# Kernel tuning notes

Hardware: AMD Instinct MI355X
Metric: run time of the kernel (lower is better)

## Reference

```python
import jax, jax.numpy as jnp
import numpy as np

B, N, D = 8, 2048, 512   # batch, ctx_size, input_size
P, H = 16, 32            # num_pers, hidden_size


def setup_inputs() -> dict:
    key = jax.random.key(0)
    k1, k2 = jax.random.split(key)
    context = jax.random.normal(k1, (B, N, D), dtype=jnp.float32)
    # stacked weights of the 16 bias-free nn.Linear(input_size, hidden_size) layers
    # xavier-uniform-style scale: sqrt(6/(fan_in+fan_out))
    limit = np.sqrt(6.0 / (D + H)).astype(np.float32)
    W = jax.random.uniform(k2, (P, H, D), dtype=jnp.float32, minval=-limit, maxval=limit)
    ctx_mask = jnp.ones((B, N), dtype=jnp.int32)
    return {"context": context, "W": W, "ctx_mask": ctx_mask}


def reference(context, W, ctx_mask):
    # per-persona projection + relu: [P, B, N, H]
    fc = jax.nn.relu(jnp.einsum('bnd,phd->pbnh', context, W))
    # sum over personas of fc @ fc^T, then average: [B, N, N]
    att = jnp.einsum('pbnh,pbmh->bnm', fc, fc) / P
    # NOTE: original uses F.softmax(attention, dim=1) -> softmax over rows (axis=1)
    att = jax.nn.softmax(att, axis=1)
    # masked_fill with markoff_value=0 on masked columns then masked rows
    m = ctx_mask.astype(att.dtype)          # [B, N]
    att = att * m[:, None, :] * m[:, :, None]
    return att
```

## Files before the change

kernel.cpp:

```cpp
#include <hip/hip_runtime.h>

#define Bc 8
#define Nc 2048
#define Dc 512
#define PH 512
#define NN 4194304

#define BM 128
#define BN 128
#define BK 32

typedef __attribute__((ext_vector_type(8))) short bf16x8;
typedef __attribute__((ext_vector_type(4))) float f32x4;

static __device__ __forceinline__ unsigned short f2b(float x) {
    union { float f; unsigned u; } v; v.f = x;
    unsigned r = v.u + 0x7fffu + ((v.u >> 16) & 1u);
    return (unsigned short)(r >> 16);
}

static __device__ __forceinline__ void load16_lds(const unsigned short* g, unsigned short* l) {
    __builtin_amdgcn_global_load_lds(
        (const __attribute__((address_space(1))) void*)g,
        (__attribute__((address_space(3))) void*)l,
        16, 0, 0);
}

__global__ __launch_bounds__(256) void prep_kernel(
    const float* __restrict__ ctx, const float* __restrict__ W,
    unsigned short* __restrict__ Xb, unsigned short* __restrict__ Wb,
    float* __restrict__ rsum) {
    int t = blockIdx.x * 256 + threadIdx.x;
    if (t < 2097152) {
        float4 v = ((const float4*)ctx)[t];
        ushort4 o;
        o.x = f2b(v.x); o.y = f2b(v.y); o.z = f2b(v.z); o.w = f2b(v.w);
        ((ushort4*)Xb)[t] = o;
    }
    if (t < 65536) {
        float4 v = ((const float4*)W)[t];
        ushort4 o;
        o.x = f2b(v.x); o.y = f2b(v.y); o.z = f2b(v.z); o.w = f2b(v.w);
        ((ushort4*)Wb)[t] = o;
    }
    if (t < 4096) {
        float4 z; z.x = 0.f; z.y = 0.f; z.z = 0.f; z.w = 0.f;
        ((float4*)rsum)[t] = z;
    }
}

__global__ __launch_bounds__(256) void gemm1_relu(
    const unsigned short* __restrict__ Xb, const unsigned short* __restrict__ Wb,
    unsigned short* __restrict__ F) {
    __shared__ unsigned short As[BM * BK];
    __shared__ unsigned short Bs[BN * BK];
    const int tid = threadIdx.x;
    const int lane = tid & 63;
    const int wave = tid >> 6;
    const int wm = wave >> 1, wn = wave & 1;
    const int row0 = blockIdx.y * BM;
    const int col0 = blockIdx.x * BN;

    f32x4 acc[4][4] = {};

    for (int k0 = 0; k0 < Dc; k0 += BK) {
#pragma unroll
        for (int j = 0; j < 2; ++j) {
            int e = j * 256 + tid;
            int rr = e >> 2, cc = e & 3;
            load16_lds(&Xb[(size_t)(row0 + rr) * Dc + k0 + cc * 8], &As[e * 8]);
            load16_lds(&Wb[(size_t)(col0 + rr) * Dc + k0 + cc * 8], &Bs[e * 8]);
        }
        __syncthreads();

        bf16x8 af[4], bfr[4];
#pragma unroll
        for (int i = 0; i < 4; ++i) {
            af[i]  = *(const bf16x8*)&As[(wm * 64 + i * 16 + (lane & 15)) * BK + (lane >> 4) * 8];
            bfr[i] = *(const bf16x8*)&Bs[(wn * 64 + i * 16 + (lane & 15)) * BK + (lane >> 4) * 8];
        }
#pragma unroll
        for (int mi = 0; mi < 4; ++mi)
#pragma unroll
            for (int ni = 0; ni < 4; ++ni)
                acc[mi][ni] = __builtin_amdgcn_mfma_f32_16x16x32_bf16(af[mi], bfr[ni], acc[mi][ni], 0, 0, 0);
        __syncthreads();
    }

#pragma unroll
    for (int mi = 0; mi < 4; ++mi) {
#pragma unroll
        for (int ni = 0; ni < 4; ++ni) {
            int col  = col0 + wn * 64 + ni * 16 + (lane & 15);
            int rowb = row0 + wm * 64 + mi * 16 + ((lane >> 4) << 2);
#pragma unroll
            for (int r = 0; r < 4; ++r) {
                float v = fmaxf(acc[mi][ni][r], 0.0f);
                F[(size_t)(rowb + r) * PH + col] = f2b(v);
            }
        }
    }
}

__global__ __launch_bounds__(256) void gemm2_rsum(
    const unsigned short* __restrict__ F, float* __restrict__ rsum) {
    __shared__ unsigned short As[BM * BK];
    __shared__ unsigned short Bs[BN * BK];
    const int tid = threadIdx.x;
    const int lane = tid & 63;
    const int wave = tid >> 6;
    const int wm = wave >> 1, wn = wave & 1;
    const int b = blockIdx.y;

    int idx = blockIdx.x;
    int j = 0;
    while (((j + 1) * (j + 2) / 2) <= idx) ++j;
    int i = idx - j * (j + 1) / 2;
    const int row0 = i * BM;
    const int col0 = j * BN;
    const unsigned short* Fb = F + (size_t)b * Nc * PH;

    f32x4 acc[4][4] = {};

    for (int k0 = 0; k0 < PH; k0 += BK) {
#pragma unroll
        for (int jj = 0; jj < 2; ++jj) {
            int e = jj * 256 + tid;
            int rr = e >> 2, cc = e & 3;
            load16_lds(&Fb[(size_t)(row0 + rr) * PH + k0 + cc * 8], &As[e * 8]);
            load16_lds(&Fb[(size_t)(col0 + rr) * PH + k0 + cc * 8], &Bs[e * 8]);
        }
        __syncthreads();

        bf16x8 af[4], bfr[4];
#pragma unroll
        for (int q = 0; q < 4; ++q) {
            af[q]  = *(const bf16x8*)&As[(wm * 64 + q * 16 + (lane & 15)) * BK + (lane >> 4) * 8];
            bfr[q] = *(const bf16x8*)&Bs[(wn * 64 + q * 16 + (lane & 15)) * BK + (lane >> 4) * 8];
        }
#pragma unroll
        for (int mi = 0; mi < 4; ++mi)
#pragma unroll
            for (int ni = 0; ni < 4; ++ni)
                acc[mi][ni] = __builtin_amdgcn_mfma_f32_16x16x32_bf16(af[mi], bfr[ni], acc[mi][ni], 0, 0, 0);
        __syncthreads();
    }

    float csum[4] = {0.f, 0.f, 0.f, 0.f};
    float rsm[4][4];
#pragma unroll
    for (int mi = 0; mi < 4; ++mi)
#pragma unroll
        for (int r = 0; r < 4; ++r) rsm[mi][r] = 0.f;

#pragma unroll
    for (int mi = 0; mi < 4; ++mi) {
#pragma unroll
        for (int ni = 0; ni < 4; ++ni) {
#pragma unroll
            for (int r = 0; r < 4; ++r) {
                float e = __expf(acc[mi][ni][r] * 0.0625f - 32.0f);
                csum[ni] += e;
                rsm[mi][r] += e;
            }
        }
    }
#pragma unroll
    for (int ni = 0; ni < 4; ++ni) {
        float s = csum[ni];
        s += __shfl_xor(s, 16);
        s += __shfl_xor(s, 32);
        if ((lane >> 4) == 0)
            atomicAdd(&rsum[b * Nc + col0 + wn * 64 + ni * 16 + lane], s);
    }
    if (i != j) {
#pragma unroll
        for (int mi = 0; mi < 4; ++mi) {
#pragma unroll
            for (int r = 0; r < 4; ++r) {
                float s = rsm[mi][r];
                s += __shfl_xor(s, 1);
                s += __shfl_xor(s, 2);
                s += __shfl_xor(s, 4);
                s += __shfl_xor(s, 8);
                if ((lane & 15) == 0)
                    atomicAdd(&rsum[b * Nc + row0 + wm * 64 + mi * 16 + ((lane >> 4) << 2) + r], s);
            }
        }
    }
}

__global__ __launch_bounds__(256) void invr_kernel(
    const float* __restrict__ rsum, const int* __restrict__ mask,
    float* __restrict__ invr) {
    int t = blockIdx.x * 256 + threadIdx.x;
    if (t < Bc * Nc) invr[t] = (float)mask[t] / rsum[t];
}

__global__ __launch_bounds__(256) void gemm2_write_sym(
    const unsigned short* __restrict__ F, const float* __restrict__ invr,
    const int* __restrict__ mask, float* __restrict__ out) {
    __shared__ unsigned short As[BM * BK];
    __shared__ unsigned short Bs[BN * BK];
    __shared__ float Ts[32 * 132];
    const int tid = threadIdx.x;
    const int lane = tid & 63;
    const int wave = tid >> 6;
    const int wm = wave >> 1, wn = wave & 1;
    const int l15 = lane & 15, q = lane >> 4;
    const int b = blockIdx.y;

    int idx = blockIdx.x;
    int j = 0;
    while (((j + 1) * (j + 2) / 2) <= idx) ++j;
    int i = idx - j * (j + 1) / 2;
    const int row0 = i * BM;
    const int col0 = j * BN;
    const unsigned short* Fb = F + (size_t)b * Nc * PH;

    f32x4 acc[4][4] = {};

    for (int k0 = 0; k0 < PH; k0 += BK) {
#pragma unroll
        for (int jj = 0; jj < 2; ++jj) {
            int e = jj * 256 + tid;
            int rr = e >> 2, cc = e & 3;
            load16_lds(&Fb[(size_t)(row0 + rr) * PH + k0 + cc * 8], &As[e * 8]);
            load16_lds(&Fb[(size_t)(col0 + rr) * PH + k0 + cc * 8], &Bs[e * 8]);
        }
        __syncthreads();

        bf16x8 af[4], bfr[4];
#pragma unroll
        for (int qq = 0; qq < 4; ++qq) {
            af[qq]  = *(const bf16x8*)&As[(wm * 64 + qq * 16 + l15) * BK + q * 8];
            bfr[qq] = *(const bf16x8*)&Bs[(wn * 64 + qq * 16 + l15) * BK + q * 8];
        }
#pragma unroll
        for (int mi = 0; mi < 4; ++mi)
#pragma unroll
            for (int ni = 0; ni < 4; ++ni)
                acc[mi][ni] = __builtin_amdgcn_mfma_f32_16x16x32_bf16(af[mi], bfr[ni], acc[mi][ni], 0, 0, 0);
        __syncthreads();
    }

#pragma unroll
    for (int mi = 0; mi < 4; ++mi)
#pragma unroll
        for (int ni = 0; ni < 4; ++ni)
#pragma unroll
            for (int r = 0; r < 4; ++r)
                acc[mi][ni][r] = __expf(acc[mi][ni][r] * 0.0625f - 32.0f);

    float* outb = out + (size_t)b * NN;

    float iv[4];
#pragma unroll
    for (int ni = 0; ni < 4; ++ni)
        iv[ni] = invr[b * Nc + col0 + wn * 64 + ni * 16 + l15];
#pragma unroll
    for (int mi = 0; mi < 4; ++mi) {
        int rowb = row0 + wm * 64 + mi * 16 + (q << 2);
        const int4 mr4 = *(const int4*)&mask[b * Nc + rowb];
        float mr[4] = {(float)mr4.x, (float)mr4.y, (float)mr4.z, (float)mr4.w};
#pragma unroll
        for (int ni = 0; ni < 4; ++ni) {
            int col = col0 + wn * 64 + ni * 16 + l15;
#pragma unroll
            for (int r = 0; r < 4; ++r)
                outb[(size_t)(rowb + r) * Nc + col] = acc[mi][ni][r] * iv[ni] * mr[r];
        }
    }

    if (i != j) {
#pragma unroll
        for (int ci = 0; ci < 4; ++ci) {
            __syncthreads();
            if (wn == (ci >> 1)) {
#pragma unroll
                for (int ni2 = 0; ni2 < 2; ++ni2) {
                    int ni = (ci & 1) * 2 + ni2;
#pragma unroll
                    for (int mi = 0; mi < 4; ++mi) {
                        *(float4*)&Ts[(ni2 * 16 + l15) * 132 + wm * 64 + mi * 16 + (q << 2)] =
                            *(float4*)&acc[mi][ni];
                    }
                }
            }
            __syncthreads();
            int cl = tid >> 3;
            int f0 = tid & 7;
            int nn = col0 + ci * 32 + cl;
            float mrow = (float)mask[b * Nc + nn];
            float* orow = &outb[(size_t)nn * Nc + row0];
#pragma unroll
            for (int g = 0; g < 4; ++g) {
                int f = f0 + g * 8;
                float4 ev  = *(float4*)&Ts[cl * 132 + 4 * f];
                float4 iv4 = *(const float4*)&invr[b * Nc + row0 + 4 * f];
                float4 o;
                o.x = ev.x * iv4.x * mrow;
                o.y = ev.y * iv4.y * mrow;
                o.z = ev.z * iv4.z * mrow;
                o.w = ev.w * iv4.w * mrow;
                *(float4*)&orow[4 * f] = o;
            }
        }
    }
}

extern "C" void kernel_launch(void* const* d_in, const int* in_sizes, int n_in,
                              void* d_out, int out_size, void* d_ws, size_t ws_size,
                              hipStream_t stream) {
    const float* ctx  = (const float*)d_in[0];
    const float* W    = (const float*)d_in[1];
    const int*   mask = (const int*)d_in[2];
    float* out = (float*)d_out;

    char* ws = (char*)d_ws;
    unsigned short* Xb = (unsigned short*)ws;
    unsigned short* Wb = (unsigned short*)(ws + 16777216);
    unsigned short* F  = (unsigned short*)(ws + 16777216 + 524288);
    float* rsum        = (float*)(ws + 16777216 + 524288 + 16777216);
    float* invr        = (float*)(ws + 16777216 + 524288 + 16777216 + 65536);

    prep_kernel<<<8192, 256, 0, stream>>>(ctx, W, Xb, Wb, rsum);
    gemm1_relu<<<dim3(4, 128), 256, 0, stream>>>(Xb, Wb, F);
    gemm2_rsum<<<dim3(136, 8), 256, 0, stream>>>(F, rsum);
    invr_kernel<<<64, 256, 0, stream>>>(rsum, mask, invr);
    gemm2_write_sym<<<dim3(136, 8), 256, 0, stream>>>(F, invr, mask, out);
}
```

Measured before the change: 251.0 us.

## Store exponentiated GEMM2 tiles to workspace instead of recomputing in second pass

The second GEMM pass, which recomputed F·Fᵀ to write normalized output, is replaced. The first pass now writes the exponentiated upper-triangular tiles in fp32 to a large workspace buffer while accumulating row and column sums. A separate scatter kernel reads them back and writes each tile plus its transpose, scaled by the inverse sums and the mask. This trades the recomputed matrix multiply for about 70 MB of extra global writes and reads, and it runs only when the workspace is large enough; otherwise the old path is used.

New measurement: 236.0 us. 1.06x faster.

```diff
diff --git a/kernel.cpp b/kernel.cpp
--- a/kernel.cpp
+++ b/kernel.cpp
@@ -5,6 +5,7 @@
 #define Dc 512
 #define PH 512
 #define NN 4194304
+#define NT 136
 
 #define BM 128
 #define BN 128
@@ -102,6 +103,164 @@
     }
 }
 
+__global__ __launch_bounds__(256) void gemm2_store(
+    const unsigned short* __restrict__ F, float* __restrict__ rsum,
+    float* __restrict__ Ework) {
+    __shared__ unsigned short As[BM * BK];
+    __shared__ unsigned short Bs[BN * BK];
+    const int tid = threadIdx.x;
+    const int lane = tid & 63;
+    const int wave = tid >> 6;
+    const int wm = wave >> 1, wn = wave & 1;
+    const int l15 = lane & 15, q = lane >> 4;
+    const int b = blockIdx.x & 7;
+    const int idx = blockIdx.x >> 3;
+
+    int j = 0;
+    while (((j + 1) * (j + 2) / 2) <= idx) ++j;
+    int i = idx - j * (j + 1) / 2;
+    const int row0 = i * BM;
+    const int col0 = j * BN;
+    const unsigned short* Fb = F + (size_t)b * Nc * PH;
+
+    f32x4 acc[4][4] = {};
+
+    for (int k0 = 0; k0 < PH; k0 += BK) {
+#pragma unroll
+        for (int jj = 0; jj < 2; ++jj) {
+            int e = jj * 256 + tid;
+            int rr = e >> 2, cc = e & 3;
+            load16_lds(&Fb[(size_t)(row0 + rr) * PH + k0 + cc * 8], &As[e * 8]);
+            load16_lds(&Fb[(size_t)(col0 + rr) * PH + k0 + cc * 8], &Bs[e * 8]);
+        }
+        __syncthreads();
+
+        bf16x8 af[4], bfr[4];
+#pragma unroll
+        for (int qq = 0; qq < 4; ++qq) {
+            af[qq]  = *(const bf16x8*)&As[(wm * 64 + qq * 16 + l15) * BK + q * 8];
+            bfr[qq] = *(const bf16x8*)&Bs[(wn * 64 + qq * 16 + l15) * BK + q * 8];
+        }
+#pragma unroll
+        for (int mi = 0; mi < 4; ++mi)
+#pragma unroll
+            for (int ni = 0; ni < 4; ++ni)
+                acc[mi][ni] = __builtin_amdgcn_mfma_f32_16x16x32_bf16(af[mi], bfr[ni], acc[mi][ni], 0, 0, 0);
+        __syncthreads();
+    }
+
+    float* Et = Ework + (size_t)(b * NT + idx) * 16384;
+
+    float csum[4] = {0.f, 0.f, 0.f, 0.f};
+    float rsm[4][4];
+#pragma unroll
+    for (int mi = 0; mi < 4; ++mi)
+#pragma unroll
+        for (int r = 0; r < 4; ++r) rsm[mi][r] = 0.f;
+
+#pragma unroll
+    for (int mi = 0; mi < 4; ++mi) {
+#pragma unroll
+        for (int ni = 0; ni < 4; ++ni) {
+#pragma unroll
+            for (int r = 0; r < 4; ++r) {
+                float e = __expf(acc[mi][ni][r] * 0.0625f - 32.0f);
+                Et[(wm * 64 + mi * 16 + (q << 2) + r) * 128 + wn * 64 + ni * 16 + l15] = e;
+                csum[ni] += e;
+                rsm[mi][r] += e;
+            }
+        }
+    }
+#pragma unroll
+    for (int ni = 0; ni < 4; ++ni) {
+        float s = csum[ni];
+        s += __shfl_xor(s, 16);
+        s += __shfl_xor(s, 32);
+        if ((lane >> 4) == 0)
+            atomicAdd(&rsum[b * Nc + col0 + wn * 64 + ni * 16 + lane], s);
+    }
+    if (i != j) {
+#pragma unroll
+        for (int mi = 0; mi < 4; ++mi) {
+#pragma unroll
+            for (int r = 0; r < 4; ++r) {
+                float s = rsm[mi][r];
+                s += __shfl_xor(s, 1);
+                s += __shfl_xor(s, 2);
+                s += __shfl_xor(s, 4);
+                s += __shfl_xor(s, 8);
+                if ((lane & 15) == 0)
+                    atomicAdd(&rsum[b * Nc + row0 + wm * 64 + mi * 16 + ((lane >> 4) << 2) + r], s);
+            }
+        }
+    }
+}
+
+__global__ __launch_bounds__(256) void invr_kernel(
+    const float* __restrict__ rsum, const int* __restrict__ mask,
+    float* __restrict__ invr) {
+    int t = blockIdx.x * 256 + threadIdx.x;
+    if (t < Bc * Nc) invr[t] = (float)mask[t] / rsum[t];
+}
+
+__global__ __launch_bounds__(256) void scatter_out(
+    const float* __restrict__ Ework, const float* __restrict__ invr,
+    const int* __restrict__ mask, float* __restrict__ out) {
+    __shared__ float Ts[32 * 132];
+    const int tid = threadIdx.x;
+    const int b = blockIdx.x & 7;
+    const int idx = blockIdx.x >> 3;
+
+    int j = 0;
+    while (((j + 1) * (j + 2) / 2) <= idx) ++j;
+    int i = idx - j * (j + 1) / 2;
+    const int row0 = i * BM;
+    const int col0 = j * BN;
+
+    const float* Et   = Ework + (size_t)(b * NT + idx) * 16384;
+    const float* invb = invr + b * Nc;
+    const int*   mb   = mask + b * Nc;
+    float* outb = out + (size_t)b * NN;
+
+    const int cl = tid >> 3, f0 = tid & 7;
+    const int mc = tid >> 1, h  = tid & 1;
+
+    for (int ci = 0; ci < 4; ++ci) {
+        if (ci) __syncthreads();
+        const int r = ci * 32 + cl;
+        const int n = row0 + r;
+        const float mrow = (float)mb[n];
+#pragma unroll
+        for (int g = 0; g < 4; ++g) {
+            int f = f0 + 8 * g;
+            float4 ev = *(const float4*)&Et[r * 128 + 4 * f];
+            *(float4*)&Ts[cl * 132 + 4 * f] = ev;
+            float4 iv = *(const float4*)&invb[col0 + 4 * f];
+            float4 o;
+            o.x = ev.x * iv.x * mrow;
+            o.y = ev.y * iv.y * mrow;
+            o.z = ev.z * iv.z * mrow;
+            o.w = ev.w * iv.w * mrow;
+            *(float4*)&outb[(size_t)n * Nc + col0 + 4 * f] = o;
+        }
+        if (i == j) continue;
+        __syncthreads();
+        const int a = col0 + mc;
+        const float mcol = (float)mb[a];
+        const int nb0 = row0 + ci * 32 + 16 * h;
+#pragma unroll
+        for (int u = 0; u < 4; ++u) {
+            float4 iv = *(const float4*)&invb[nb0 + 4 * u];
+            float4 o;
+            o.x = Ts[(16 * h + 4 * u + 0) * 132 + mc] * iv.x * mcol;
+            o.y = Ts[(16 * h + 4 * u + 1) * 132 + mc] * iv.y * mcol;
+            o.z = Ts[(16 * h + 4 * u + 2) * 132 + mc] * iv.z * mcol;
+            o.w = Ts[(16 * h + 4 * u + 3) * 132 + mc] * iv.w * mcol;
+            *(float4*)&outb[(size_t)a * Nc + nb0 + 4 * u] = o;
+        }
+    }
+}
+
 __global__ __launch_bounds__(256) void gemm2_rsum(
     const unsigned short* __restrict__ F, float* __restrict__ rsum) {
     __shared__ unsigned short As[BM * BK];
@@ -188,13 +347,6 @@
             }
         }
     }
-}
-
-__global__ __launch_bounds__(256) void invr_kernel(
-    const float* __restrict__ rsum, const int* __restrict__ mask,
-    float* __restrict__ invr) {
-    int t = blockIdx.x * 256 + threadIdx.x;
-    if (t < Bc * Nc) invr[t] = (float)mask[t] / rsum[t];
 }
 
 __global__ __launch_bounds__(256) void gemm2_write_sym(
@@ -318,15 +470,33 @@
     float* out = (float*)d_out;
 
     char* ws = (char*)d_ws;
-    unsigned short* Xb = (unsigned short*)ws;
-    unsigned short* Wb = (unsigned short*)(ws + 16777216);
-    unsigned short* F  = (unsigned short*)(ws + 16777216 + 524288);
-    float* rsum        = (float*)(ws + 16777216 + 524288 + 16777216);
-    float* invr        = (float*)(ws + 16777216 + 524288 + 16777216 + 65536);
-
-    prep_kernel<<<8192, 256, 0, stream>>>(ctx, W, Xb, Wb, rsum);
-    gemm1_relu<<<dim3(4, 128), 256, 0, stream>>>(Xb, Wb, F);
-    gemm2_rsum<<<dim3(136, 8), 256, 0, stream>>>(F, rsum);
-    invr_kernel<<<64, 256, 0, stream>>>(rsum, mask, invr);
-    gemm2_write_sym<<<dim3(136, 8), 256, 0, stream>>>(F, invr, mask, out);
-}
+
+    const size_t NEED = 88211456;
+
+    if (ws_size >= NEED) {
+        float*          Ework = (float*)ws;
+        unsigned short* Xb    = (unsigned short*)ws;
+        unsigned short* Wb    = (unsigned short*)(ws + 16777216);
+        unsigned short* F     = (unsigned short*)(ws + 71303168);
+        float*          rsum  = (float*)(ws + 88080384);
+        float*          invr  = (float*)(ws + 88145920);
+
+        prep_kernel<<<8192, 256, 0, stream>>>(ctx, W, Xb, Wb, rsum);
+        gemm1_relu<<<dim3(4, 128), 256, 0, stream>>>(Xb, Wb, F);
+        gemm2_store<<<1088, 256, 0, stream>>>(F, rsum, Ework);
+        invr_kernel<<<64, 256, 0, stream>>>(rsum, mask, invr);
+        scatter_out<<<1088, 256, 0, stream>>>(Ework, invr, mask, out);
+    } else {
+        unsigned short* Xb = (unsigned short*)ws;
+        unsigned short* Wb = (unsigned short*)(ws + 16777216);
+        unsigned short* F  = (unsigned short*)(ws + 16777216 + 524288);
+        float* rsum        = (float*)(ws + 16777216 + 524288 + 16777216);
+        float* invr        = (float*)(ws + 16777216 + 524288 + 16777216 + 65536);
+
+        prep_kernel<<<8192, 256, 0, stream>>>(ctx, W, Xb, Wb, rsum);
+        gemm1_relu<<<dim3(4, 128), 256, 0, stream>>>(Xb, Wb, F);
+        gemm2_rsum<<<dim3(136, 8), 256, 0, stream>>>(F, rsum);
+        invr_kernel<<<64, 256, 0, stream>>>(rsum, mask, invr);
+        gemm2_write_sym<<<dim3(136, 8), 256, 0, stream>>>(F, invr, mask, out);
+    }
+}
```
